# Performance work log

Measured on AMD Instinct MI355X. Metric: run time of the kernel, lower is better.

## Reference

```python
import jax, jax.numpy as jnp
import numpy as np

SMOOTHNESS_RATIO = 0.2
DEGREE_RATIO = 0.1
SPARSITY_RATIO = 0.1
VERY_SMALL_NUMBER = 1e-12


def setup_inputs() -> dict:
    key = jax.random.key(0)
    k1, k2 = jax.random.split(key)
    B, N, D = 64, 1024, 16
    out_adj = jax.random.uniform(k1, (B, N, N), dtype=jnp.float32)  # nonneg adjacency (softmax-like)
    features = jax.random.normal(k2, (B, N, D), dtype=jnp.float32)
    return {"out_adj": out_adj, "features": features}


def reference(out_adj, features):
    # Faithful fused version of add_batch_graph_loss with keep_batch_dim=True.
    # Per sample i: smoothness_ratio * tr(F^T (diag(deg) - A) F) / (N*N)
    #   tr(F^T diag(deg) F) = sum_n deg_n ||f_n||^2
    #   tr(F^T A F)        = sum(F * (A @ F))
    B, N, _ = out_adj.shape
    denom = jnp.float32(N * N)

    deg = jnp.sum(out_adj, axis=-1)                       # [B, N] row degrees
    AF = jnp.einsum('bij,bjd->bid', out_adj, features)    # [B, N, D]
    smooth = (jnp.einsum('bn,bnd->b', deg, features * features)
              - jnp.einsum('bnd,bnd->b', features, AF))   # [B] = tr(F^T L F)
    graph_loss = SMOOTHNESS_RATIO * smooth / denom

    # degree regularization: -degree_ratio * ones^T log(A @ ones + eps) / N
    # A @ ones == deg
    log_degrees = jnp.log(deg + VERY_SMALL_NUMBER)        # [B, N]
    graph_loss = graph_loss - DEGREE_RATIO * jnp.sum(log_degrees, axis=-1) / N

    # sparsity: sparsity_ratio * sum(A^2) / (N*N)
    graph_loss = graph_loss + SPARSITY_RATIO * jnp.sum(out_adj * out_adj, axis=(1, 2)) / denom
    return graph_loss  # [B]
```

## Files before the change

kernel.cpp:

```cpp
#include <hip/hip_runtime.h>


#define NN      1024
#define DD      16
#define ROWS    64
#define TPB     512
#define GRPS    128
#define SMOOTHR 0.2f
#define DEGRR   0.1f
#define SPARSR  0.1f
#define EPSV    1e-12f

typedef float vf4 __attribute__((ext_vector_type(4)));
typedef float vf2 __attribute__((ext_vector_type(2)));

__global__ __launch_bounds__(TPB, 4)
void graph_loss_kernel(const float* __restrict__ A,
                       const float* __restrict__ F,
                       float* __restrict__ out) {
    __shared__ float degq[ROWS][GRPS + 1];
    __shared__ float wred[8][2];

    const int tid = threadIdx.x;
    const int bid = blockIdx.x;
    const int b   = bid >> 4;
    const int n0  = (bid & 15) * ROWS;

    const float* __restrict__ Fb = F + (size_t)b * NN * DD;
    const float* __restrict__ Ab = A + ((size_t)b * NN + n0) * NN;

    vf4 w[2][4];
    #pragma unroll
    for (int jj = 0; jj < 2; ++jj)
        #pragma unroll
        for (int q = 0; q < 4; ++q)
            w[jj][q] = (vf4){0.f, 0.f, 0.f, 0.f};

    float sq = 0.f;
    const float* __restrict__ arow = Ab + 2 * tid;
    const int  g       = tid >> 2;
    const bool deglane = (tid & 3) == 0;

    #define LOADR(r) __builtin_nontemporal_load((const vf2*)(arow + (size_t)(r) * NN))
    #define LDF(dst, rr)                                                     \
        do {                                                                 \
            const vf4* __restrict__ Fr =                                     \
                (const vf4*)(Fb + (size_t)(n0 + (rr)) * DD);                 \
            dst##0 = Fr[0]; dst##1 = Fr[1]; dst##2 = Fr[2]; dst##3 = Fr[3];  \
        } while (0)
    #define COMPUTE(av, f0v, f1v, f2v, f3v, rr)                              \
        do {                                                                 \
            float s_ = av.x + av.y;                                          \
            s_ += __shfl_xor(s_, 1);                                         \
            s_ += __shfl_xor(s_, 2);                                         \
            if (deglane) degq[(rr)][g] = s_;                                 \
            sq += av.x * av.x + av.y * av.y;                                 \
            w[0][0] += av.x * f0v;  w[1][0] += av.y * f0v;                   \
            w[0][1] += av.x * f1v;  w[1][1] += av.y * f1v;                   \
            w[0][2] += av.x * f2v;  w[1][2] += av.y * f2v;                   \
            w[0][3] += av.x * f3v;  w[1][3] += av.y * f3v;                   \
        } while (0)

    vf2 a0 = LOADR(0);
    vf2 a1 = LOADR(1);
    vf2 a2 = LOADR(2);
    vf2 a3 = LOADR(3);
    vf4 fA0, fA1, fA2, fA3, fB0, fB1, fB2, fB3;
    LDF(fA, 0);

    #pragma unroll 1
    for (int r = 0; r < ROWS - 4; r += 4) {
        LDF(fB, r + 1);
        COMPUTE(a0, fA0, fA1, fA2, fA3, r);
        a0 = LOADR(r + 4);
        LDF(fA, r + 2);
        COMPUTE(a1, fB0, fB1, fB2, fB3, r + 1);
        a1 = LOADR(r + 5);
        LDF(fB, r + 3);
        COMPUTE(a2, fA0, fA1, fA2, fA3, r + 2);
        a2 = LOADR(r + 6);
        LDF(fA, r + 4);
        COMPUTE(a3, fB0, fB1, fB2, fB3, r + 3);
        a3 = LOADR(r + 7);
    }
    LDF(fB, ROWS - 3);
    COMPUTE(a0, fA0, fA1, fA2, fA3, ROWS - 4);
    LDF(fA, ROWS - 2);
    COMPUTE(a1, fB0, fB1, fB2, fB3, ROWS - 3);
    LDF(fB, ROWS - 1);
    COMPUTE(a2, fA0, fA1, fA2, fA3, ROWS - 2);
    COMPUTE(a3, fB0, fB1, fB2, fB3, ROWS - 1);

    #undef LOADR
    #undef LDF
    #undef COMPUTE

    __syncthreads();
    float lg = 0.f, dfn = 0.f;
    if (tid < ROWS) {
        float s = 0.f;
        #pragma unroll 1
        for (int i = 0; i < GRPS; ++i) s += degq[tid][i];
        lg = logf(s + EPSV);
        const float* p = Fb + (size_t)(n0 + tid) * DD;
        float t = 0.f;
        #pragma unroll
        for (int q = 0; q < 4; ++q) {
            const vf4 f = *(const vf4*)(p + 4 * q);
            t += f.x * f.x + f.y * f.y + f.z * f.z + f.w * f.w;
        }
        dfn = s * t;
    }

    float dot = 0.f;
    {
        const float* p = Fb + (size_t)(2 * tid) * DD;
        #pragma unroll
        for (int jj = 0; jj < 2; ++jj)
            #pragma unroll
            for (int q = 0; q < 4; ++q) {
                const vf4 f = *(const vf4*)(p + jj * DD + 4 * q);
                dot += f.x * w[jj][q].x + f.y * w[jj][q].y
                     + f.z * w[jj][q].z + f.w * w[jj][q].w;
            }
    }

    #pragma unroll
    for (int m = 1; m < 64; m <<= 1) {
        dot += __shfl_xor(dot, m);
        sq  += __shfl_xor(sq, m);
        lg  += __shfl_xor(lg, m);
        dfn += __shfl_xor(dfn, m);
    }
    const int wv = tid >> 6;
    if ((tid & 63) == 0) { wred[wv][0] = dot; wred[wv][1] = sq; }
    __syncthreads();
    if (tid == 0) {
        float Dt = 0.f, Q = 0.f;
        #pragma unroll
        for (int i = 0; i < 8; ++i) { Dt += wred[i][0]; Q += wred[i][1]; }
        const float denom = (float)NN * (float)NN;
        const float contrib = SMOOTHR * (dfn - Dt) / denom
                            - DEGRR * lg / (float)NN
                            + SPARSR * Q / denom;
        atomicAdd(out + b, contrib);
    }
}

extern "C" void kernel_launch(void* const* d_in, const int* in_sizes, int n_in,
                              void* d_out, int out_size, void* d_ws, size_t ws_size,
                              hipStream_t stream) {
    const float* A = (const float*)d_in[0];
    const float* F = (const float*)d_in[1];
    float* out = (float*)d_out;

    const int B = out_size;
    (void)hipMemsetAsync(d_out, 0, (size_t)B * sizeof(float), stream);
    graph_loss_kernel<<<dim3(B * (NN / ROWS)), dim3(TPB), 0, stream>>>(A, F, out);
}
```

Before: 365.8 us.

## Raise occupancy bound, use DPP quad reduction, drop nontemporal loads, scalarize accumulators

Doubles the launch-bounds occupancy hint from 4 to 8 blocks per CU, which caps register use. The quad shuffle reduction becomes DPP row permutes, the nontemporal hint on adjacency loads is removed, and the vector accumulators are split into scalar arrays. The degree sum is unrolled with four partial sums. The tighter register cap risks spilling, and removing the nontemporal hint changes how the streamed data interacts with the cache.

```diff
diff --git a/kernel.cpp b/kernel.cpp
--- a/kernel.cpp
+++ b/kernel.cpp
@@ -14,7 +14,7 @@
 typedef float vf4 __attribute__((ext_vector_type(4)));
 typedef float vf2 __attribute__((ext_vector_type(2)));
 
-__global__ __launch_bounds__(TPB, 4)
+__global__ __launch_bounds__(TPB, 8)
 void graph_loss_kernel(const float* __restrict__ A,
                        const float* __restrict__ F,
                        float* __restrict__ out) {
@@ -29,36 +29,51 @@
     const float* __restrict__ Fb = F + (size_t)b * NN * DD;
     const float* __restrict__ Ab = A + ((size_t)b * NN + n0) * NN;
 
-    vf4 w[2][4];
+    float w0[16], w1[16];
     #pragma unroll
-    for (int jj = 0; jj < 2; ++jj)
-        #pragma unroll
-        for (int q = 0; q < 4; ++q)
-            w[jj][q] = (vf4){0.f, 0.f, 0.f, 0.f};
+    for (int k = 0; k < 16; ++k) { w0[k] = 0.f; w1[k] = 0.f; }
 
     float sq = 0.f;
     const float* __restrict__ arow = Ab + 2 * tid;
     const int  g       = tid >> 2;
     const bool deglane = (tid & 3) == 0;
 
-    #define LOADR(r) __builtin_nontemporal_load((const vf2*)(arow + (size_t)(r) * NN))
+    #define LOADR(r) (*(const vf2*)(arow + (size_t)(r) * NN))
     #define LDF(dst, rr)                                                     \
         do {                                                                 \
             const vf4* __restrict__ Fr =                                     \
                 (const vf4*)(Fb + (size_t)(n0 + (rr)) * DD);                 \
             dst##0 = Fr[0]; dst##1 = Fr[1]; dst##2 = Fr[2]; dst##3 = Fr[3];  \
         } while (0)
+    #define QUADRED(s_)                                                      \
+        do {                                                                 \
+            s_ += __builtin_bit_cast(float, __builtin_amdgcn_update_dpp(     \
+                0, __builtin_bit_cast(int, s_), 0xB1, 0xF, 0xF, true));      \
+            s_ += __builtin_bit_cast(float, __builtin_amdgcn_update_dpp(     \
+                0, __builtin_bit_cast(int, s_), 0x4E, 0xF, 0xF, true));      \
+        } while (0)
     #define COMPUTE(av, f0v, f1v, f2v, f3v, rr)                              \
         do {                                                                 \
             float s_ = av.x + av.y;                                          \
-            s_ += __shfl_xor(s_, 1);                                         \
-            s_ += __shfl_xor(s_, 2);                                         \
+            QUADRED(s_);                                                     \
             if (deglane) degq[(rr)][g] = s_;                                 \
             sq += av.x * av.x + av.y * av.y;                                 \
-            w[0][0] += av.x * f0v;  w[1][0] += av.y * f0v;                   \
-            w[0][1] += av.x * f1v;  w[1][1] += av.y * f1v;                   \
-            w[0][2] += av.x * f2v;  w[1][2] += av.y * f2v;                   \
-            w[0][3] += av.x * f3v;  w[1][3] += av.y * f3v;                   \
+            w0[0]  += av.x * f0v.x;  w1[0]  += av.y * f0v.x;                 \
+            w0[1]  += av.x * f0v.y;  w1[1]  += av.y * f0v.y;                 \
+            w0[2]  += av.x * f0v.z;  w1[2]  += av.y * f0v.z;                 \
+            w0[3]  += av.x * f0v.w;  w1[3]  += av.y * f0v.w;                 \
+            w0[4]  += av.x * f1v.x;  w1[4]  += av.y * f1v.x;                 \
+            w0[5]  += av.x * f1v.y;  w1[5]  += av.y * f1v.y;                 \
+            w0[6]  += av.x * f1v.z;  w1[6]  += av.y * f1v.z;                 \
+            w0[7]  += av.x * f1v.w;  w1[7]  += av.y * f1v.w;                 \
+            w0[8]  += av.x * f2v.x;  w1[8]  += av.y * f2v.x;                 \
+            w0[9]  += av.x * f2v.y;  w1[9]  += av.y * f2v.y;                 \
+            w0[10] += av.x * f2v.z;  w1[10] += av.y * f2v.z;                 \
+            w0[11] += av.x * f2v.w;  w1[11] += av.y * f2v.w;                 \
+            w0[12] += av.x * f3v.x;  w1[12] += av.y * f3v.x;                 \
+            w0[13] += av.x * f3v.y;  w1[13] += av.y * f3v.y;                 \
+            w0[14] += av.x * f3v.z;  w1[14] += av.y * f3v.z;                 \
+            w0[15] += av.x * f3v.w;  w1[15] += av.y * f3v.w;                 \
         } while (0)
 
     vf2 a0 = LOADR(0);
@@ -93,14 +108,21 @@
 
     #undef LOADR
     #undef LDF
+    #undef QUADRED
     #undef COMPUTE
 
     __syncthreads();
     float lg = 0.f, dfn = 0.f;
     if (tid < ROWS) {
-        float s = 0.f;
-        #pragma unroll 1
-        for (int i = 0; i < GRPS; ++i) s += degq[tid][i];
+        float s0 = 0.f, s1 = 0.f, s2 = 0.f, s3 = 0.f;
+        #pragma unroll
+        for (int i = 0; i < GRPS / 4; ++i) {
+            s0 += degq[tid][4 * i + 0];
+            s1 += degq[tid][4 * i + 1];
+            s2 += degq[tid][4 * i + 2];
+            s3 += degq[tid][4 * i + 3];
+        }
+        const float s = (s0 + s1) + (s2 + s3);
         lg = logf(s + EPSV);
         const float* p = Fb + (size_t)(n0 + tid) * DD;
         float t = 0.f;
@@ -114,15 +136,17 @@
 
     float dot = 0.f;
     {
-        const float* p = Fb + (size_t)(2 * tid) * DD;
+        const vf4* __restrict__ P = (const vf4*)(Fb + (size_t)(2 * tid) * DD);
         #pragma unroll
-        for (int jj = 0; jj < 2; ++jj)
-            #pragma unroll
-            for (int q = 0; q < 4; ++q) {
-                const vf4 f = *(const vf4*)(p + jj * DD + 4 * q);
-                dot += f.x * w[jj][q].x + f.y * w[jj][q].y
-                     + f.z * w[jj][q].z + f.w * w[jj][q].w;
-            }
+        for (int q = 0; q < 4; ++q) {
+            const vf4 f = P[q];
+            dot += f.x * w0[4*q] + f.y * w0[4*q+1] + f.z * w0[4*q+2] + f.w * w0[4*q+3];
+        }
+        #pragma unroll
+        for (int q = 0; q < 4; ++q) {
+            const vf4 f = P[4 + q];
+            dot += f.x * w1[4*q] + f.y * w1[4*q+1] + f.z * w1[4*q+2] + f.w * w1[4*q+3];
+        }
     }
 
     #pragma unroll
```

Result: slower. 392.9 us (+7.4%).
